# Performance work log

Hardware: AMD Instinct MI355X
Metric: run time of the kernel (lower is better)

Reference implementation:

```python
import jax, jax.numpy as jnp
import numpy as np

NEG_INF = -1e12  # matches masked_fill value -1000000000000.0
LEAKY_SLOPE = 0.2


def setup_inputs() -> dict:
    key = jax.random.key(0)
    k1, k2, k3, k4, k5 = jax.random.split(key, 5)
    B, C, H, N, F_IN, F_OUT = 4, 4, 4, 1024, 64, 64
    h = jax.random.normal(k1, (B, C, N, F_IN), dtype=jnp.float32)
    adj = jax.random.randint(k2, (B, N, N), 0, 2).astype(jnp.float32)
    w = jax.random.normal(k3, (C, H, F_IN, F_OUT), dtype=jnp.float32) * 0.1
    a_src = jax.random.normal(k4, (C, H, F_OUT, 1), dtype=jnp.float32) * 0.1
    a_dst = jax.random.normal(k5, (C, H, F_OUT, 1), dtype=jnp.float32) * 0.1
    return {"h": h, "adj": adj, "w": w, "a_src": a_src, "a_dst": a_dst}


def reference(h, adj, w, a_src, a_dst):
    # h: [B,C,N,f_in], w: [C,H,f_in,f_out] -> h_prime: [B,C,H,N,f_out]
    h_prime = jnp.einsum('bcnf,chfo->bchno', h, w)
    t = jnp.tanh(h_prime)
    # additive attention scores: [B,C,H,N]
    attn_src = jnp.einsum('bchno,cho->bchn', t, a_src[..., 0])
    attn_dst = jnp.einsum('bchno,cho->bchn', t, a_dst[..., 0])
    # attn[b,c,h,i,j] = src[i] + dst[j]  -> [B,C,H,N,N]
    attn = attn_src[..., :, None] + attn_dst[..., None, :]
    attn = jnp.where(attn >= 0, attn, LEAKY_SLOPE * attn)  # leaky_relu(0.2)
    N = h.shape[2]
    adj_sl = adj + jnp.eye(N, dtype=adj.dtype)  # add self-loops
    mask = (adj_sl == 0)[:, None, None, :, :]   # [B,1,1,N,N]
    attn = jnp.where(mask, NEG_INF, attn)
    attn = jax.nn.softmax(attn, axis=-1)
    # dropout is identity (attn_dropout=0.0 / eval mode)
    out = jnp.einsum('bchnm,bchmo->bchno', attn, h_prime)
    return out
```

## Files before the change

### kernel.cpp

```cpp
#include <hip/hip_runtime.h>
#include <hip/hip_bf16.h>
#include <math.h>

#define NB 4
#define NC 4
#define NH 4
#define NN 1024
#define NF 64
#define NCOMBO 64
#define LEAK 0.2f

typedef __attribute__((ext_vector_type(8)))  short  short8;
typedef __attribute__((ext_vector_type(16))) float  float16;

static __device__ __forceinline__ unsigned pk_bf16(float a, float b) {
    union { __hip_bfloat162 h; unsigned u; } cv;
    cv.h = __float22bfloat162_rn(make_float2(a, b));
    return cv.u;
}

static __device__ __forceinline__ float fast_tanh(float x) {
    const float e = __expf(2.f * x);
    return 1.f - 2.f * __builtin_amdgcn_rcpf(1.f + e);
}

static __device__ __forceinline__ void async_cp16(const void* gsrc, void* ldst) {
    __builtin_amdgcn_global_load_lds(
        (const __attribute__((address_space(1))) unsigned int*)gsrc,
        (__attribute__((address_space(3))) unsigned int*)ldst, 16, 0, 0);
}

__global__ __launch_bounds__(256) void k1_hprime(
    const float* __restrict__ h, const float* __restrict__ w,
    const float* __restrict__ a_src, const float* __restrict__ a_dst,
    unsigned short* __restrict__ hpt, float* __restrict__ asrc,
    float* __restrict__ adst)
{
    __shared__ __align__(16) char ovr[64*65*4];
    __shared__ float w_s[NF*NF];
    __shared__ float as_lds[NF], ad_lds[NF];
    float* hT = (float*)ovr;

    const int g    = blockIdx.x >> 4;
    const int tile = blockIdx.x & 15;
    const int b = g >> 4, c = (g >> 2) & 3, hh = g & 3;
    const int t = threadIdx.x;
    const int tr = t >> 4, tc = t & 15;

    const float4* wsrc = (const float4*)(w + ((size_t)(c*NH + hh))*NF*NF);
    #pragma unroll
    for (int i = 0; i < 4; ++i)
        ((float4*)w_s)[t + i*256] = wsrc[t + i*256];
    if (t < NF) {
        as_lds[t] = a_src[(c*NH + hh)*NF + t];
        ad_lds[t] = a_dst[(c*NH + hh)*NF + t];
    }
    const float* hsrc = h + (((size_t)(b*NC + c))*NN + tile*64)*NF;
    #pragma unroll
    for (int i = 0; i < 4; ++i) {
        const int r = (t >> 4) + i*16, f4 = (t & 15)*4;
        const float4 v = *(const float4*)&hsrc[r*NF + f4];
        hT[(f4+0)*65 + r] = v.x; hT[(f4+1)*65 + r] = v.y;
        hT[(f4+2)*65 + r] = v.z; hT[(f4+3)*65 + r] = v.w;
    }
    __syncthreads();

    float acc[4][4] = {{0.f}};
    #pragma unroll 8
    for (int f = 0; f < 64; ++f) {
        const float4 hv = *(const float4*)&hT[f*65 + tr*4];
        const float4 wv = *(const float4*)&w_s[f*64 + tc*4];
        acc[0][0] = fmaf(hv.x, wv.x, acc[0][0]);
        acc[0][1] = fmaf(hv.x, wv.y, acc[0][1]);
        acc[0][2] = fmaf(hv.x, wv.z, acc[0][2]);
        acc[0][3] = fmaf(hv.x, wv.w, acc[0][3]);
        acc[1][0] = fmaf(hv.y, wv.x, acc[1][0]);
        acc[1][1] = fmaf(hv.y, wv.y, acc[1][1]);
        acc[1][2] = fmaf(hv.y, wv.z, acc[1][2]);
        acc[1][3] = fmaf(hv.y, wv.w, acc[1][3]);
        acc[2][0] = fmaf(hv.z, wv.x, acc[2][0]);
        acc[2][1] = fmaf(hv.z, wv.y, acc[2][1]);
        acc[2][2] = fmaf(hv.z, wv.z, acc[2][2]);
        acc[2][3] = fmaf(hv.z, wv.w, acc[2][3]);
        acc[3][0] = fmaf(hv.w, wv.x, acc[3][0]);
        acc[3][1] = fmaf(hv.w, wv.y, acc[3][1]);
        acc[3][2] = fmaf(hv.w, wv.z, acc[3][2]);
        acc[3][3] = fmaf(hv.w, wv.w, acc[3][3]);
    }

    float ps[4] = {0.f,0.f,0.f,0.f}, pd[4] = {0.f,0.f,0.f,0.f};
    #pragma unroll
    for (int r = 0; r < 4; ++r)
        #pragma unroll
        for (int cc = 0; cc < 4; ++cc) {
            const float tt = fast_tanh(acc[r][cc]);
            ps[r] = fmaf(tt, as_lds[tc*4+cc], ps[r]);
            pd[r] = fmaf(tt, ad_lds[tc*4+cc], pd[r]);
        }
    __syncthreads();
    float* redS = (float*)ovr;
    float* redD = redS + 1024;
    #pragma unroll
    for (int r = 0; r < 4; ++r) {
        redS[(tr*4+r)*16 + tc] = ps[r];
        redD[(tr*4+r)*16 + tc] = pd[r];
    }
    __syncthreads();
    if (t < 64) {
        float4 s0 = *(const float4*)&redS[t*16],     s1 = *(const float4*)&redS[t*16+4];
        float4 s2 = *(const float4*)&redS[t*16+8],   s3 = *(const float4*)&redS[t*16+12];
        asrc[(size_t)g*NN + tile*64 + t] =
            (s0.x+s0.y+s0.z+s0.w) + (s1.x+s1.y+s1.z+s1.w) +
            (s2.x+s2.y+s2.z+s2.w) + (s3.x+s3.y+s3.z+s3.w);
        float4 d0 = *(const float4*)&redD[t*16],     d1 = *(const float4*)&redD[t*16+4];
        float4 d2 = *(const float4*)&redD[t*16+8],   d3 = *(const float4*)&redD[t*16+12];
        adst[(size_t)g*NN + tile*64 + t] =
            (d0.x+d0.y+d0.z+d0.w) + (d1.x+d1.y+d1.z+d1.w) +
            (d2.x+d2.y+d2.z+d2.w) + (d3.x+d3.y+d3.z+d3.w);
    }
    #pragma unroll
    for (int cc = 0; cc < 4; ++cc) {
        const int o = tc*4 + cc;
        const int pos = (((((tr>>2)*2 + (o>>5))*2 + ((tr>>1)&1))*32 + (o&31))*8)
                        + (tr&1)*4;
        uint2 pk;
        pk.x = pk_bf16(acc[0][cc], acc[1][cc]);
        pk.y = pk_bf16(acc[2][cc], acc[3][cc]);
        *(uint2*)&hpt[((size_t)g*16 + tile)*4096 + pos] = pk;
    }
}

__global__ __launch_bounds__(256) void k2_bits(
    const float* __restrict__ adj, unsigned long long* __restrict__ bits)
{
    const int idx = blockIdx.x*256 + threadIdx.x;
    const int j  = idx & (NN-1);
    const int i  = (idx >> 10) & (NN-1);
    const int bb = idx >> 20;
    const float av = adj[idx];
    const bool pred = (av != 0.f) || (j == i);
    const unsigned long long m = __ballot(pred);
    if ((j & 63) == 0) bits[((size_t)bb*NN + i)*(NN/64) + (j >> 6)] = m;
}

__global__ __launch_bounds__(256, 4) void k3_attn(
    const unsigned short* __restrict__ hpt, const float* __restrict__ asrc,
    const float* __restrict__ adst, const unsigned long long* __restrict__ bits,
    float* __restrict__ out)
{
    __shared__ float edP[NN];
    __shared__ float edN[NN];
    __shared__ float src_lds[64];
    __shared__ float ps_buf[64];
    __shared__ float red_lds[4];
    __shared__ unsigned long long bits_lds[64*17];
    __shared__ __align__(16) char ovraw[17408];
    unsigned short* fragB = (unsigned short*)ovraw;
    float* comb = (float*)ovraw;

    const int g  = blockIdx.x & 63;
    const int it = blockIdx.x >> 6;
    const int b  = g >> 4;
    const int t  = threadIdx.x;
    const int i0 = it*64;
    const int w = t >> 6, lane = t & 63;
    const int l31 = lane & 31, half = lane >> 5;
    const int rg = w >> 1, jh = w & 1;
    const int myrow = rg*32 + l31;

    {
        const char* gs = (const char*)hpt + ((size_t)g*16 + 0)*8192 + w*2048 + lane*16;
        char* ls = ovraw + w*2048;
        async_cp16(gs, ls);
        async_cp16(gs + 1024, ls + 1024);
    }

    float mx = -1e30f;
    #pragma unroll
    for (int q = 0; q < 4; ++q) {
        const float d = adst[(size_t)g*NN + q*256 + t];
        edP[q*256 + t] = __expf(d);
        edN[q*256 + t] = __expf(LEAK*d);
        mx = fmaxf(mx, d);
    }
    if (t < 64) src_lds[t] = asrc[(size_t)g*NN + i0 + t];
    {
        const unsigned long long* bsrc = bits + ((size_t)b*NN + i0)*16;
        #pragma unroll
        for (int q = 0; q < 4; ++q) {
            const int idx = q*256 + t;
            bits_lds[(idx >> 4)*17 + (idx & 15)] = bsrc[idx];
        }
    }
    #pragma unroll
    for (int off = 32; off > 0; off >>= 1) mx = fmaxf(mx, __shfl_down(mx, off));
    if (lane == 0) red_lds[w] = mx;
    __syncthreads();
    const float maxdst = fmaxf(fmaxf(red_lds[0], red_lds[1]),
                               fmaxf(red_lds[2], red_lds[3]));

    const float sv  = src_lds[myrow];
    const float s0  = sv + maxdst;
    const float mi  = fmaxf(s0, LEAK*s0);
    const float esP = __expf(sv - mi);
    const float esN = __expf(LEAK*sv - mi);

    float16 acc0, acc1;
    #pragma unroll
    for (int i = 0; i < 16; ++i) { acc0[i] = 0.f; acc1[i] = 0.f; }
    float psum = 0.f;

    for (int jt = 0; jt < 16; ++jt) {
        __syncthreads();
        const int fb = jt & 1;
        if (jt < 15) {
            const char* gs = (const char*)hpt + ((size_t)g*16 + jt + 1)*8192
                             + w*2048 + lane*16;
            char* ls = ovraw + (fb ^ 1)*8192 + w*2048;
            async_cp16(gs, ls);
            async_cp16(gs + 1024, ls + 1024);
        }
        const unsigned long long wb = bits_lds[myrow*17 + jt];

        #pragma unroll
        for (int kk = 0; kk < 2; ++kk) {
            const int ks = jh*2 + kk;
            const int jb = jt*64 + ks*16 + half*8;
            const float4 P0 = *(const float4*)&edP[jb];
            const float4 P1 = *(const float4*)&edP[jb + 4];
            const float4 N0 = *(const float4*)&edN[jb];
            const float4 N1 = *(const float4*)&edN[jb + 4];
            const unsigned bb = (unsigned)(wb >> (ks*16 + half*8)) & 0xffu;

            float p0, p1, p2, p3, p4, p5, p6, p7;
            p0 = fmaxf(P0.x*esP, N0.x*esN); p0 = (bb & 1u)   ? p0 : 0.f;
            p1 = fmaxf(P0.y*esP, N0.y*esN); p1 = (bb & 2u)   ? p1 : 0.f;
            p2 = fmaxf(P0.z*esP, N0.z*esN); p2 = (bb & 4u)   ? p2 : 0.f;
            p3 = fmaxf(P0.w*esP, N0.w*esN); p3 = (bb & 8u)   ? p3 : 0.f;
            p4 = fmaxf(P1.x*esP, N1.x*esN); p4 = (bb & 16u)  ? p4 : 0.f;
            p5 = fmaxf(P1.y*esP, N1.y*esN); p5 = (bb & 32u)  ? p5 : 0.f;
            p6 = fmaxf(P1.z*esP, N1.z*esN); p6 = (bb & 64u)  ? p6 : 0.f;
            p7 = fmaxf(P1.w*esP, N1.w*esN); p7 = (bb & 128u) ? p7 : 0.f;
            psum += ((p0 + p1) + (p2 + p3)) + ((p4 + p5) + (p6 + p7));

            union { short8 v; unsigned u[4]; } af;
            af.u[0] = pk_bf16(p0, p1);
            af.u[1] = pk_bf16(p2, p3);
            af.u[2] = pk_bf16(p4, p5);
            af.u[3] = pk_bf16(p6, p7);

            const short8 b0 = *(const short8*)
                &fragB[fb*4096 + (((ks*2 + 0)*2 + half)*32 + l31)*8];
            const short8 b1 = *(const short8*)
                &fragB[fb*4096 + (((ks*2 + 1)*2 + half)*32 + l31)*8];
            acc0 = __builtin_amdgcn_mfma_f32_32x32x16_bf16(af.v, b0, acc0, 0, 0, 0);
            acc1 = __builtin_amdgcn_mfma_f32_32x32x16_bf16(af.v, b1, acc1, 0, 0, 0);
        }
    }

    psum += __shfl_xor(psum, 32);
    __syncthreads();

    if (jh == 1) {
        float* cb = comb + (rg*64 + lane)*34;
        #pragma unroll
        for (int i = 0; i < 8; ++i) {
            float2 v0; v0.x = acc0[2*i]; v0.y = acc0[2*i+1];
            float2 v1; v1.x = acc1[2*i]; v1.y = acc1[2*i+1];
            *(float2*)&cb[2*i]      = v0;
            *(float2*)&cb[16 + 2*i] = v1;
        }
        if (lane < 32) ps_buf[rg*32 + l31] = psum;
    }
    __syncthreads();
    if (jh == 0) {
        const float* cb = comb + (rg*64 + lane)*34;
        #pragma unroll
        for (int i = 0; i < 8; ++i) {
            const float2 v0 = *(const float2*)&cb[2*i];
            const float2 v1 = *(const float2*)&cb[16 + 2*i];
            acc0[2*i] += v0.x; acc0[2*i+1] += v0.y;
            acc1[2*i] += v1.x; acc1[2*i+1] += v1.y;
        }
        psum += ps_buf[rg*32 + l31];
        if (lane < 32) ps_buf[rg*32 + l31] = psum;
    }
    __syncthreads();
    if (jh == 0) {
        #pragma unroll
        for (int reg = 0; reg < 16; ++reg) {
            const int r = (reg & 3) + 8*(reg >> 2) + 4*half;
            const float inv = __builtin_amdgcn_rcpf(ps_buf[rg*32 + r]);
            const size_t base = ((size_t)g*NN + i0 + rg*32 + r)*NF;
            out[base + l31]      = acc0[reg] * inv;
            out[base + l31 + 32] = acc1[reg] * inv;
        }
    }
}

extern "C" void kernel_launch(void* const* d_in, const int* in_sizes, int n_in,
                              void* d_out, int out_size, void* d_ws, size_t ws_size,
                              hipStream_t stream)
{
    const float* h     = (const float*)d_in[0];
    const float* adj   = (const float*)d_in[1];
    const float* w     = (const float*)d_in[2];
    const float* a_src = (const float*)d_in[3];
    const float* a_dst = (const float*)d_in[4];
    float* out = (float*)d_out;

    char* ws = (char*)d_ws;
    unsigned short* hpt  = (unsigned short*)ws;
    float* asrc          = (float*)(ws + 8388608);
    float* adst          = (float*)(ws + 8388608 + 262144);
    unsigned long long* bits = (unsigned long long*)(ws + 8388608 + 524288);

    k1_hprime<<<dim3(NCOMBO*16), dim3(256), 0, stream>>>(h, w, a_src, a_dst, hpt, asrc, adst);
    k2_bits  <<<dim3(NB*NN*NN/256), dim3(256), 0, stream>>>(adj, bits);
    k3_attn  <<<dim3(1024), dim3(256), 0, stream>>>(hpt, asrc, adst, bits, out);
}
```

Before: 133.3 us.

## Fuse adjacency bitmask into producer kernel and simplify attention softmax path

Folds the adjacency-to-bitmask pass into the h_prime producer kernel, cutting three launches to two. The producer now writes exp(dst) and exp(0.2*dst) tables directly. The attention kernel drops its per-block max reduction and instead applies a per-row factor exp((LEAK-1)*src), whose scaling cancels in the softmax normalization. The attention kernel also drops async LDS double-buffering of the bf16 h_prime tiles and reads MFMA B fragments and exp tables straight from global/L2, and both grids use a swizzled block order. In exchange the unshifted exponentials risk overflow for large scores, and the direct global fragment loads depend on cache hits.

```diff
diff --git a/kernel.cpp b/kernel.cpp
--- a/kernel.cpp
+++ b/kernel.cpp
@@ -24,27 +24,25 @@
     return 1.f - 2.f * __builtin_amdgcn_rcpf(1.f + e);
 }
 
-static __device__ __forceinline__ void async_cp16(const void* gsrc, void* ldst) {
-    __builtin_amdgcn_global_load_lds(
-        (const __attribute__((address_space(1))) unsigned int*)gsrc,
-        (__attribute__((address_space(3))) unsigned int*)ldst, 16, 0, 0);
-}
-
-__global__ __launch_bounds__(256) void k1_hprime(
-    const float* __restrict__ h, const float* __restrict__ w,
-    const float* __restrict__ a_src, const float* __restrict__ a_dst,
+__global__ __launch_bounds__(256) void gA_produce(
+    const float* __restrict__ h, const float* __restrict__ adj,
+    const float* __restrict__ w, const float* __restrict__ a_src,
+    const float* __restrict__ a_dst,
     unsigned short* __restrict__ hpt, float* __restrict__ asrc,
-    float* __restrict__ adst)
+    float* __restrict__ edPt, float* __restrict__ edNt,
+    unsigned long long* __restrict__ bits)
 {
-    __shared__ __align__(16) char ovr[64*65*4];
-    __shared__ float w_s[NF*NF];
-    __shared__ float as_lds[NF], ad_lds[NF];
-    float* hT = (float*)ovr;
-
-    const int g    = blockIdx.x >> 4;
-    const int tile = blockIdx.x & 15;
+    __shared__ __align__(16) char smem[33536];
+    float* hT     = (float*)smem;
+    float* w_s    = (float*)(smem + 16640);
+    float* as_lds = (float*)(smem + 33024);
+    float* ad_lds = (float*)(smem + 33280);
+
+    const int idx  = blockIdx.x;
+    const int t    = threadIdx.x;
+    const int g    = (idx & 7)*8 + ((idx >> 3) & 7);
+    const int tile = idx >> 6;
     const int b = g >> 4, c = (g >> 2) & 3, hh = g & 3;
-    const int t = threadIdx.x;
     const int tr = t >> 4, tc = t & 15;
 
     const float4* wsrc = (const float4*)(w + ((size_t)(c*NH + hh))*NF*NF);
@@ -98,7 +96,7 @@
             pd[r] = fmaf(tt, ad_lds[tc*4+cc], pd[r]);
         }
     __syncthreads();
-    float* redS = (float*)ovr;
+    float* redS = (float*)smem;
     float* redD = redS + 1024;
     #pragma unroll
     for (int r = 0; r < 4; ++r) {
@@ -107,16 +105,18 @@
     }
     __syncthreads();
     if (t < 64) {
-        float4 s0 = *(const float4*)&redS[t*16],     s1 = *(const float4*)&redS[t*16+4];
-        float4 s2 = *(const float4*)&redS[t*16+8],   s3 = *(const float4*)&redS[t*16+12];
+        float4 s0 = *(const float4*)&redS[t*16],   s1 = *(const float4*)&redS[t*16+4];
+        float4 s2 = *(const float4*)&redS[t*16+8], s3 = *(const float4*)&redS[t*16+12];
         asrc[(size_t)g*NN + tile*64 + t] =
             (s0.x+s0.y+s0.z+s0.w) + (s1.x+s1.y+s1.z+s1.w) +
             (s2.x+s2.y+s2.z+s2.w) + (s3.x+s3.y+s3.z+s3.w);
-        float4 d0 = *(const float4*)&redD[t*16],     d1 = *(const float4*)&redD[t*16+4];
-        float4 d2 = *(const float4*)&redD[t*16+8],   d3 = *(const float4*)&redD[t*16+12];
-        adst[(size_t)g*NN + tile*64 + t] =
+        float4 d0 = *(const float4*)&redD[t*16],   d1 = *(const float4*)&redD[t*16+4];
+        float4 d2 = *(const float4*)&redD[t*16+8], d3 = *(const float4*)&redD[t*16+12];
+        const float dsum =
             (d0.x+d0.y+d0.z+d0.w) + (d1.x+d1.y+d1.z+d1.w) +
             (d2.x+d2.y+d2.z+d2.w) + (d3.x+d3.y+d3.z+d3.w);
+        edPt[(size_t)g*NN + tile*64 + t] = __expf(dsum);
+        edNt[(size_t)g*NN + tile*64 + t] = __expf(LEAK*dsum);
     }
     #pragma unroll
     for (int cc = 0; cc < 4; ++cc) {
@@ -128,119 +128,93 @@
         pk.y = pk_bf16(acc[2][cc], acc[3][cc]);
         *(uint2*)&hpt[((size_t)g*16 + tile)*4096 + pos] = pk;
     }
-}
-
-__global__ __launch_bounds__(256) void k2_bits(
-    const float* __restrict__ adj, unsigned long long* __restrict__ bits)
+
+    {
+        const int base = idx*4096;
+        #pragma unroll
+        for (int q = 0; q < 16; ++q) {
+            const int e  = base + q*256 + t;
+            const int j  = e & (NN-1);
+            const int i  = (e >> 10) & (NN-1);
+            const int bb = e >> 20;
+            const bool pred = (adj[e] != 0.f) || (j == i);
+            const unsigned long long m = __ballot(pred);
+            if ((t & 63) == 0) bits[((size_t)bb*NN + i)*16 + (j >> 6)] = m;
+        }
+    }
+}
+
+__global__ __launch_bounds__(256, 4) void gC_attn(
+    const unsigned short* __restrict__ hpt, const float* __restrict__ asrc,
+    const float* __restrict__ edPt, const float* __restrict__ edNt,
+    const unsigned long long* __restrict__ bits, float* __restrict__ out)
 {
-    const int idx = blockIdx.x*256 + threadIdx.x;
-    const int j  = idx & (NN-1);
-    const int i  = (idx >> 10) & (NN-1);
-    const int bb = idx >> 20;
-    const float av = adj[idx];
-    const bool pred = (av != 0.f) || (j == i);
-    const unsigned long long m = __ballot(pred);
-    if ((j & 63) == 0) bits[((size_t)bb*NN + i)*(NN/64) + (j >> 6)] = m;
-}
-
-__global__ __launch_bounds__(256, 4) void k3_attn(
-    const unsigned short* __restrict__ hpt, const float* __restrict__ asrc,
-    const float* __restrict__ adst, const unsigned long long* __restrict__ bits,
-    float* __restrict__ out)
-{
-    __shared__ float edP[NN];
-    __shared__ float edN[NN];
-    __shared__ float src_lds[64];
-    __shared__ float ps_buf[64];
-    __shared__ float red_lds[4];
-    __shared__ unsigned long long bits_lds[64*17];
-    __shared__ __align__(16) char ovraw[17408];
-    unsigned short* fragB = (unsigned short*)ovraw;
-    float* comb = (float*)ovraw;
-
-    const int g  = blockIdx.x & 63;
-    const int it = blockIdx.x >> 6;
-    const int b  = g >> 4;
-    const int t  = threadIdx.x;
-    const int i0 = it*64;
-    const int w = t >> 6, lane = t & 63;
+    __shared__ __align__(16) char smem[26368];
+    unsigned long long* bits_lds = (unsigned long long*)smem;
+    float* comb   = (float*)(smem + 8704);
+    float* ps_buf = (float*)(smem + 26112);
+
+    const int idx = blockIdx.x;
+    const int t   = threadIdx.x;
+    const int g   = (idx & 7)*8 + ((idx >> 3) & 7);
+    const int it  = idx >> 6;
+    const int b   = g >> 4;
+    const int i0  = it*64;
+    const int wv = t >> 6, lane = t & 63;
     const int l31 = lane & 31, half = lane >> 5;
-    const int rg = w >> 1, jh = w & 1;
+    const int rg = wv >> 1, jh = wv & 1;
     const int myrow = rg*32 + l31;
 
-    {
-        const char* gs = (const char*)hpt + ((size_t)g*16 + 0)*8192 + w*2048 + lane*16;
-        char* ls = ovraw + w*2048;
-        async_cp16(gs, ls);
-        async_cp16(gs + 1024, ls + 1024);
-    }
-
-    float mx = -1e30f;
-    #pragma unroll
-    for (int q = 0; q < 4; ++q) {
-        const float d = adst[(size_t)g*NN + q*256 + t];
-        edP[q*256 + t] = __expf(d);
-        edN[q*256 + t] = __expf(LEAK*d);
-        mx = fmaxf(mx, d);
-    }
-    if (t < 64) src_lds[t] = asrc[(size_t)g*NN + i0 + t];
     {
         const unsigned long long* bsrc = bits + ((size_t)b*NN + i0)*16;
         #pragma unroll
         for (int q = 0; q < 4; ++q) {
-            const int idx = q*256 + t;
-            bits_lds[(idx >> 4)*17 + (idx & 15)] = bsrc[idx];
-        }
-    }
-    #pragma unroll
-    for (int off = 32; off > 0; off >>= 1) mx = fmaxf(mx, __shfl_down(mx, off));
-    if (lane == 0) red_lds[w] = mx;
-    __syncthreads();
-    const float maxdst = fmaxf(fmaxf(red_lds[0], red_lds[1]),
-                               fmaxf(red_lds[2], red_lds[3]));
-
-    const float sv  = src_lds[myrow];
-    const float s0  = sv + maxdst;
-    const float mi  = fmaxf(s0, LEAK*s0);
-    const float esP = __expf(sv - mi);
-    const float esN = __expf(LEAK*sv - mi);
+            const int e = q*256 + t;
+            bits_lds[(e >> 4)*17 + (e & 15)] = bsrc[e];
+        }
+    }
+    __syncthreads();
+
+    const float sv    = asrc[(size_t)g*NN + i0 + myrow];
+    const float ratio = __expf((LEAK - 1.f)*sv);
 
     float16 acc0, acc1;
     #pragma unroll
     for (int i = 0; i < 16; ++i) { acc0[i] = 0.f; acc1[i] = 0.f; }
     float psum = 0.f;
 
+    const float* tbP = edPt + (size_t)g*NN;
+    const float* tbN = edNt + (size_t)g*NN;
+    const unsigned short* hq0 = hpt + (size_t)g*16*4096;
+
+    #pragma unroll 2
     for (int jt = 0; jt < 16; ++jt) {
-        __syncthreads();
-        const int fb = jt & 1;
-        if (jt < 15) {
-            const char* gs = (const char*)hpt + ((size_t)g*16 + jt + 1)*8192
-                             + w*2048 + lane*16;
-            char* ls = ovraw + (fb ^ 1)*8192 + w*2048;
-            async_cp16(gs, ls);
-            async_cp16(gs + 1024, ls + 1024);
-        }
         const unsigned long long wb = bits_lds[myrow*17 + jt];
+        const float* tP = tbP + jt*64;
+        const float* tN = tbN + jt*64;
+        const unsigned short* hq = hq0 + jt*4096;
 
         #pragma unroll
         for (int kk = 0; kk < 2; ++kk) {
             const int ks = jh*2 + kk;
-            const int jb = jt*64 + ks*16 + half*8;
-            const float4 P0 = *(const float4*)&edP[jb];
-            const float4 P1 = *(const float4*)&edP[jb + 4];
-            const float4 N0 = *(const float4*)&edN[jb];
-            const float4 N1 = *(const float4*)&edN[jb + 4];
-            const unsigned bb = (unsigned)(wb >> (ks*16 + half*8)) & 0xffu;
+            const int jo = ks*16 + half*8;
+            const float4 P0 = *(const float4*)&tP[jo];
+            const float4 P1 = *(const float4*)&tP[jo + 4];
+            const float4 N0 = *(const float4*)&tN[jo];
+            const float4 N1 = *(const float4*)&tN[jo + 4];
+            const short8 b0 = *(const short8*)&hq[(((ks*2 + 0)*2 + half)*32 + l31)*8];
+            const short8 b1 = *(const short8*)&hq[(((ks*2 + 1)*2 + half)*32 + l31)*8];
+            const unsigned bb = (unsigned)(wb >> jo) & 0xffu;
 
             float p0, p1, p2, p3, p4, p5, p6, p7;
-            p0 = fmaxf(P0.x*esP, N0.x*esN); p0 = (bb & 1u)   ? p0 : 0.f;
-            p1 = fmaxf(P0.y*esP, N0.y*esN); p1 = (bb & 2u)   ? p1 : 0.f;
-            p2 = fmaxf(P0.z*esP, N0.z*esN); p2 = (bb & 4u)   ? p2 : 0.f;
-            p3 = fmaxf(P0.w*esP, N0.w*esN); p3 = (bb & 8u)   ? p3 : 0.f;
-            p4 = fmaxf(P1.x*esP, N1.x*esN); p4 = (bb & 16u)  ? p4 : 0.f;
-            p5 = fmaxf(P1.y*esP, N1.y*esN); p5 = (bb & 32u)  ? p5 : 0.f;
-            p6 = fmaxf(P1.z*esP, N1.z*esN); p6 = (bb & 64u)  ? p6 : 0.f;
-            p7 = fmaxf(P1.w*esP, N1.w*esN); p7 = (bb & 128u) ? p7 : 0.f;
+            p0 = fmaxf(P0.x, ratio*N0.x); p0 = (bb & 1u)   ? p0 : 0.f;
+            p1 = fmaxf(P0.y, ratio*N0.y); p1 = (bb & 2u)   ? p1 : 0.f;
+            p2 = fmaxf(P0.z, ratio*N0.z); p2 = (bb & 4u)   ? p2 : 0.f;
+            p3 = fmaxf(P0.w, ratio*N0.w); p3 = (bb & 8u)   ? p3 : 0.f;
+            p4 = fmaxf(P1.x, ratio*N1.x); p4 = (bb & 16u)  ? p4 : 0.f;
+            p5 = fmaxf(P1.y, ratio*N1.y); p5 = (bb & 32u)  ? p5 : 0.f;
+            p6 = fmaxf(P1.z, ratio*N1.z); p6 = (bb & 64u)  ? p6 : 0.f;
+            p7 = fmaxf(P1.w, ratio*N1.w); p7 = (bb & 128u) ? p7 : 0.f;
             psum += ((p0 + p1) + (p2 + p3)) + ((p4 + p5) + (p6 + p7));
 
             union { short8 v; unsigned u[4]; } af;
@@ -249,10 +223,6 @@
             af.u[2] = pk_bf16(p4, p5);
             af.u[3] = pk_bf16(p6, p7);
 
-            const short8 b0 = *(const short8*)
-                &fragB[fb*4096 + (((ks*2 + 0)*2 + half)*32 + l31)*8];
-            const short8 b1 = *(const short8*)
-                &fragB[fb*4096 + (((ks*2 + 1)*2 + half)*32 + l31)*8];
             acc0 = __builtin_amdgcn_mfma_f32_32x32x16_bf16(af.v, b0, acc0, 0, 0, 0);
             acc1 = __builtin_amdgcn_mfma_f32_32x32x16_bf16(af.v, b1, acc1, 0, 0, 0);
         }
@@ -310,12 +280,14 @@
     float* out = (float*)d_out;
 
     char* ws = (char*)d_ws;
-    unsigned short* hpt  = (unsigned short*)ws;
-    float* asrc          = (float*)(ws + 8388608);
-    float* adst          = (float*)(ws + 8388608 + 262144);
-    unsigned long long* bits = (unsigned long long*)(ws + 8388608 + 524288);
-
-    k1_hprime<<<dim3(NCOMBO*16), dim3(256), 0, stream>>>(h, w, a_src, a_dst, hpt, asrc, adst);
-    k2_bits  <<<dim3(NB*NN*NN/256), dim3(256), 0, stream>>>(adj, bits);
-    k3_attn  <<<dim3(1024), dim3(256), 0, stream>>>(hpt, asrc, adst, bits, out);
-}
+    unsigned short* hpt = (unsigned short*)ws;
+    float* asrc         = (float*)(ws + 8388608);
+    float* edP          = (float*)(ws + 8388608 + 262144);
+    float* edN          = (float*)(ws + 8388608 + 524288);
+    unsigned long long* bits = (unsigned long long*)(ws + 8388608 + 786432);
+
+    gA_produce<<<dim3(1024), dim3(256), 0, stream>>>(
+        h, adj, w, a_src, a_dst, hpt, asrc, edP, edN, bits);
+    gC_attn<<<dim3(1024), dim3(256), 0, stream>>>(
+        hpt, asrc, edP, edN, bits, out);
+}
```

Measured after the change: 143.0 us. +7.3%, slower.
